# Kernel tuning notes

Measured on AMD Instinct MI355X. Metric: run time of the kernel, lower is better.

The kernel has to match this reference:

```python
import jax, jax.numpy as jnp
import numpy as np

GRID = 64            # volume_pixel per axis
VOX = 1.0 / GRID     # voxel_physical (unit-cube volume_physical)
CHUNK = 128          # gaussians per scan step


def _voxel_centers():
    # [V,3] centers of voxels of a unit cube, V = GRID**3
    c = (jnp.arange(GRID, dtype=jnp.float32) + 0.5) * VOX
    zz, yy, xx = jnp.meshgrid(c, c, c, indexing='ij')
    return jnp.stack([xx.ravel(), yy.ravel(), zz.ravel()], axis=-1)


def _quat_to_rotmat(q):
    # q: [N,4] (w,x,y,z), normalized -> [N,3,3]
    q = q / jnp.linalg.norm(q, axis=-1, keepdims=True)
    w, x, y, z = q[:, 0], q[:, 1], q[:, 2], q[:, 3]
    return jnp.stack([
        jnp.stack([1 - 2 * (y * y + z * z), 2 * (x * y - w * z), 2 * (x * z + w * y)], -1),
        jnp.stack([2 * (x * y + w * z), 1 - 2 * (x * x + z * z), 2 * (y * z - w * x)], -1),
        jnp.stack([2 * (x * z - w * y), 2 * (y * z + w * x), 1 - 2 * (x * x + y * y)], -1),
    ], axis=-2)


def _voxelize(means3D, densities, scales, rotations):
    N = means3D.shape[0]
    R = _quat_to_rotmat(rotations)                       # [N,3,3]
    inv_s2 = 1.0 / (scales * scales)                     # [N,3]
    # Sigma^{-1} = R diag(1/s^2) R^T
    Sinv = jnp.einsum('nij,nj,nkj->nik', R, inv_s2, R)   # [N,3,3]
    centers = _voxel_centers()                            # [V,3]
    n_chunks = N // CHUNK
    mu_c = means3D.reshape(n_chunks, CHUNK, 3)
    de_c = densities.reshape(n_chunks, CHUNK)
    Si_c = Sinv.reshape(n_chunks, CHUNK, 3, 3)

    def step(vol, xs):
        mu, dens, Si = xs
        d = centers[None, :, :] - mu[:, None, :]                 # [C,V,3]
        qf = jnp.einsum('cvi,cij,cvj->cv', d, Si, d)             # [C,V]
        vol = vol + jnp.sum(dens[:, None] * jnp.exp(-0.5 * qf), axis=0)
        return vol, None

    vol0 = jnp.zeros((GRID ** 3,), dtype=means3D.dtype)
    volume, _ = jax.lax.scan(step, vol0, (mu_c, de_c, Si_c))
    volume = volume.reshape(GRID, GRID, GRID)
    # screen-space-style radius: 3 sigma of the largest axis, in voxels
    radii = jnp.ceil(3.0 * jnp.max(scales, axis=-1) / VOX).astype(jnp.int32)
    return volume, radii


def setup_inputs() -> dict:
    key = jax.random.key(0)
    k1, k2, k3, k4 = jax.random.split(key, 4)
    N = 4096
    means3D = jax.random.uniform(k1, (N, 3), dtype=jnp.float32)                 # in unit cube
    densities = jax.random.uniform(k2, (N,), dtype=jnp.float32)
    scales = jax.random.uniform(k3, (N, 3), dtype=jnp.float32) * 0.05 + 0.01    # 0.6-3.8 voxels
    rotations = jax.random.normal(k4, (N, 4), dtype=jnp.float32)
    return {"means3D": means3D, "densities": densities, "scales": scales, "rotations": rotations}


def reference(means3D, densities, scales, rotations):
    return _voxelize(means3D, densities, scales, rotations)
```

## Files before the change

kernel.cpp:

```cpp
#include <hip/hip_runtime.h>

#define GRIDN 64
#define NVOX (GRIDN * GRIDN * GRIDN)
#define VOXF (1.0f / 64.0f)
#define QCUT 16.0f
#define EXPSCL (-0.72134752044f)
#define SKIPTH (QCUT * EXPSCL)

#define WS_CULLA 0
#define WS_CULLB (4 * 4096)
#define WS_REC   (8 * 4096)

__global__ __launch_bounds__(256) void prep_kernel(
    const float* __restrict__ means, const float* __restrict__ dens,
    const float* __restrict__ scales, const float* __restrict__ rots,
    float* __restrict__ ws, float* __restrict__ radii_out, int N)
{
    int i = blockIdx.x * 256 + threadIdx.x;
    if (i >= N) return;

    float qw = rots[i * 4 + 0], qx = rots[i * 4 + 1];
    float qy = rots[i * 4 + 2], qz = rots[i * 4 + 3];
    float inm = rsqrtf(qw * qw + qx * qx + qy * qy + qz * qz);
    qw *= inm; qx *= inm; qy *= inm; qz *= inm;
    float r00 = 1.f - 2.f * (qy * qy + qz * qz);
    float r01 = 2.f * (qx * qy - qw * qz);
    float r02 = 2.f * (qx * qz + qw * qy);
    float r10 = 2.f * (qx * qy + qw * qz);
    float r11 = 1.f - 2.f * (qx * qx + qz * qz);
    float r12 = 2.f * (qy * qz - qw * qx);
    float r20 = 2.f * (qx * qz - qw * qy);
    float r21 = 2.f * (qy * qz + qw * qx);
    float r22 = 1.f - 2.f * (qx * qx + qy * qy);

    float s0 = scales[i * 3 + 0], s1 = scales[i * 3 + 1], s2 = scales[i * 3 + 2];
    float v0 = s0 * s0, v1 = s1 * s1, v2 = s2 * s2;
    float i0 = 1.f / v0, i1 = 1.f / v1, i2 = 1.f / v2;

    float A = (r00 * r00 * i0 + r01 * r01 * i1 + r02 * r02 * i2) * EXPSCL;
    float B = (r10 * r10 * i0 + r11 * r11 * i1 + r12 * r12 * i2) * EXPSCL;
    float C = (r20 * r20 * i0 + r21 * r21 * i1 + r22 * r22 * i2) * EXPSCL;
    float D = (r00 * r10 * i0 + r01 * r11 * i1 + r02 * r12 * i2) * EXPSCL;
    float E = (r00 * r20 * i0 + r01 * r21 * i1 + r02 * r22 * i2) * EXPSCL;
    float F = (r10 * r20 * i0 + r11 * r21 * i1 + r12 * r22 * i2) * EXPSCL;

    float Cxx = r00 * r00 * v0 + r01 * r01 * v1 + r02 * r02 * v2;
    float Cyy = r10 * r10 * v0 + r11 * r11 * v1 + r12 * r12 * v2;
    float Czz = r20 * r20 * v0 + r21 * r21 * v1 + r22 * r22 * v2;

    float de = fmaxf(dens[i], 1e-30f);
    float qeff = fmaxf(QCUT + 2.0f * logf(de), 0.0f);
    float smax2 = fmaxf(v0, fmaxf(v1, v2));

    float mx = means[i * 3 + 0], my = means[i * 3 + 1], mz = means[i * 3 + 2];
    float4 ca; ca.x = mx; ca.y = my; ca.z = mz; ca.w = sqrtf(qeff * Cxx);
    float4 cb; cb.x = sqrtf(qeff * Cyy); cb.y = sqrtf(qeff * Czz);
    cb.z = qeff * smax2; cb.w = 0.f;
    ((float4*)(ws + WS_CULLA))[i] = ca;
    ((float4*)(ws + WS_CULLB))[i] = cb;

    float4* R = (float4*)(ws + WS_REC + (size_t)i * 16);
    float4 w0; w0.x = A; w0.y = B; w0.z = C; w0.w = 2.f * D;
    float4 w1; w1.x = 2.f * E; w1.y = 2.f * F; w1.z = -0.25f / A; w1.w = log2f(de);
    float4 w2; w2.x = mx; w2.y = my; w2.z = mz; w2.w = 0.f;
    R[0] = w0; R[1] = w1; R[2] = w2;

    float m = fmaxf(s0, fmaxf(s1, s2));
    radii_out[i] = ceilf(m * 3.0f * 64.0f);

    if (i == 0) {
        float4 zv; zv.x = 0.f; zv.y = 0.f; zv.z = 0.f; zv.w = 0.f;
        float4 d1; d1.x = 0.f; d1.y = 0.f; d1.z = 0.f; d1.w = -1e30f;
        float4* Dm = (float4*)(ws + WS_REC + (size_t)N * 16);
        Dm[0] = zv; Dm[1] = d1; Dm[2] = zv;
    }
}

__global__ __launch_bounds__(1024, 8) void vox_kernel(
    const float* __restrict__ ws, float* __restrict__ out, int N)
{
    __shared__ unsigned long long cmask[64];
    __shared__ int slist[3072];
    __shared__ float4 sreq[3][256];
    __shared__ float4 plds[16][64];

    const float* rec = ws + WS_REC;
    const int tid = threadIdx.x;
    const int lane = tid & 63, wave = tid >> 6;
    const int t = (blockIdx.x * 341) & 511;
    const int tX = t & 7, tY = (t >> 3) & 7, tZ = t >> 6;
    const int x0 = tX << 3;
    const int y = (tY << 3) + (lane & 7);
    const int z = (tZ << 3) + (lane >> 3);
    const float px = (x0 + 0.5f) * VOXF;
    const float py = (y + 0.5f) * VOXF;
    const float pz = (z + 0.5f) * VOXF;

    const float lox = (x0 + 0.5f) * VOXF,          hix = (x0 + 7.5f) * VOXF;
    const float loy = ((tY << 3) + 0.5f) * VOXF,   hiy = ((tY << 3) + 7.5f) * VOXF;
    const float loz = ((tZ << 3) + 0.5f) * VOXF,   hiz = ((tZ << 3) + 7.5f) * VOXF;

    const int nch = (N + 63) >> 6;
    #pragma unroll
    for (int k = 0; k < 4; ++k) {
        const int c = (k << 4) | wave;
        unsigned long long bal = 0ull;
        if (c < nch) {
            const int gi = (c << 6) + lane;
            const int gc = gi < N ? gi : N - 1;
            float4 ca = ((const float4*)(ws + WS_CULLA))[gc];
            float4 cb = ((const float4*)(ws + WS_CULLB))[gc];
            float cx = fminf(fmaxf(ca.x, lox), hix) - ca.x;
            float cy = fminf(fmaxf(ca.y, loy), hiy) - ca.y;
            float cz = fminf(fmaxf(ca.z, loz), hiz) - ca.z;
            float d2 = fmaf(cx, cx, fmaf(cy, cy, cz * cz));
            bool keep = (gi < N) && (d2 <= cb.z)
                && (ca.x + ca.w >= lox) && (ca.x - ca.w <= hix)
                && (ca.y + cb.x >= loy) && (ca.y - cb.x <= hiy)
                && (ca.z + cb.y >= loz) && (ca.z - cb.y <= hiz);
            bal = __ballot(keep);
        }
        if (lane == 0) cmask[c] = bal;
    }
    __syncthreads();

    unsigned long long mk = cmask[lane];
    int pc = __popcll(mk);
    int incl = pc;
    #pragma unroll
    for (int d = 1; d < 64; d <<= 1) {
        int t2 = __shfl_up(incl, d, 64);
        if (lane >= d) incl += t2;
    }
    const int excl = incl - pc;
    int cnt = __builtin_amdgcn_readlane(incl, 63);
    if (cnt > 3072) cnt = 3072;

    #pragma unroll
    for (int k = 0; k < 4; ++k) {
        const int c = (k << 4) | wave;
        unsigned long long mc = cmask[c];
        if (mc == 0ull) continue;
        int bse = __builtin_amdgcn_readlane(excl, c);
        if ((mc >> lane) & 1ull) {
            int pre = __popcll(mc & ((1ull << lane) - 1ull));
            int pos = bse + pre;
            if (pos < 3072) slist[pos] = (c << 6) + lane;
        }
    }
    int padend = ((cnt + 255) >> 8) << 8;
    if (padend > 3072) padend = 3072;
    for (int i = cnt + tid; i < padend; i += 1024) slist[i] = N;
    __syncthreads();

    float4 accL, accH;
    accL.x = accL.y = accL.z = accL.w = 0.f;
    accH = accL;

    for (int base = 0; base < padend; base += 256) {
        if (tid < 768) {
            const int part = tid >> 8, s = tid & 255;
            const int gi = slist[base + s];
            sreq[part][s] = ((const float4*)(rec + ((size_t)gi << 4)))[part];
        }
        __syncthreads();

        const int s0 = wave << 4;
        #pragma unroll 4
        for (int j = 0; j < 16; ++j) {
            float4 a0 = sreq[0][s0 + j];
            float4 a1 = sreq[1][s0 + j];
            float4 a2 = sreq[2][s0 + j];
            float dy = py - a2.y, dz = pz - a2.z;
            float tt  = fmaf(a1.y, dy, a0.z * dz);
            float qyz = fmaf(a0.y * dy, dy, fmaf(tt, dz, a1.w));
            float gx  = fmaf(a0.w, dy, a1.x * dz);
            float qmx = fmaf(gx * gx, a1.z, qyz);
            if (!__all(qmx < SKIPTH)) {
                float dx0 = px - a2.x;
                float dx1 = dx0 + VOXF,        dx2 = dx0 + 2.f * VOXF;
                float dx3 = dx0 + 3.f * VOXF,  dx4 = dx0 + 4.f * VOXF;
                float dx5 = dx0 + 5.f * VOXF,  dx6 = dx0 + 6.f * VOXF;
                float dx7 = dx0 + 7.f * VOXF;
                accL.x += __builtin_amdgcn_exp2f(fmaf(dx0, fmaf(a0.x, dx0, gx), qyz));
                accL.y += __builtin_amdgcn_exp2f(fmaf(dx1, fmaf(a0.x, dx1, gx), qyz));
                accL.z += __builtin_amdgcn_exp2f(fmaf(dx2, fmaf(a0.x, dx2, gx), qyz));
                accL.w += __builtin_amdgcn_exp2f(fmaf(dx3, fmaf(a0.x, dx3, gx), qyz));
                accH.x += __builtin_amdgcn_exp2f(fmaf(dx4, fmaf(a0.x, dx4, gx), qyz));
                accH.y += __builtin_amdgcn_exp2f(fmaf(dx5, fmaf(a0.x, dx5, gx), qyz));
                accH.z += __builtin_amdgcn_exp2f(fmaf(dx6, fmaf(a0.x, dx6, gx), qyz));
                accH.w += __builtin_amdgcn_exp2f(fmaf(dx7, fmaf(a0.x, dx7, gx), qyz));
            }
        }
        __syncthreads();
    }

    const int v = (z << 12) + (y << 6) + x0;

    plds[wave][lane] = accL;
    __syncthreads();
    if (wave == 0) {
        float4 r = plds[0][lane];
        #pragma unroll
        for (int w = 1; w < 16; ++w) {
            float4 p = plds[w][lane];
            r.x += p.x; r.y += p.y; r.z += p.z; r.w += p.w;
        }
        *(float4*)&out[v] = r;
    }
    __syncthreads();
    plds[wave][lane] = accH;
    __syncthreads();
    if (wave == 0) {
        float4 r = plds[0][lane];
        #pragma unroll
        for (int w = 1; w < 16; ++w) {
            float4 p = plds[w][lane];
            r.x += p.x; r.y += p.y; r.z += p.z; r.w += p.w;
        }
        *(float4*)&out[v + 4] = r;
    }
}

extern "C" void kernel_launch(void* const* d_in, const int* in_sizes, int n_in,
                              void* d_out, int out_size, void* d_ws, size_t ws_size,
                              hipStream_t stream)
{
    const float* means  = (const float*)d_in[0];
    const float* dens   = (const float*)d_in[1];
    const float* scales = (const float*)d_in[2];
    const float* rots   = (const float*)d_in[3];
    float* out = (float*)d_out;
    float* ws  = (float*)d_ws;
    const int N = in_sizes[1];

    prep_kernel<<<(N + 255) / 256, 256, 0, stream>>>(means, dens, scales, rots,
                                                     ws, out + NVOX, N);
    vox_kernel<<<512, 1024, 0, stream>>>(ws, out, N);
}
```

Measured before the change: 27.60 us.

## Fuse Gaussian preprocessing into voxel kernel, recomputing cull and quadric params per block

Drops the separate prep kernel and its workspace. Each block recomputes each Gaussian's culling bounds from the raw inputs during the cull phase, and rebuilds the quadric coefficients for the surviving Gaussians when staging them into shared memory. Radii output is written by the first 16 blocks. This removes one kernel launch and a global round trip. The cost is redundant per-block math: all 4096 cull parameter sets are recomputed in each of 512 blocks, and the staging of each 256-Gaussian batch now runs on 256 threads instead of 768.

```diff
diff --git a/kernel.cpp b/kernel.cpp
--- a/kernel.cpp
+++ b/kernel.cpp
@@ -7,84 +7,45 @@
 #define EXPSCL (-0.72134752044f)
 #define SKIPTH (QCUT * EXPSCL)
 
-#define WS_CULLA 0
-#define WS_CULLB (4 * 4096)
-#define WS_REC   (8 * 4096)
-
-__global__ __launch_bounds__(256) void prep_kernel(
+
+#define CULL_PARAMS(gc_, mx_, my_, mz_, rx_, ry_, rz_, sph_) do {              \
+    float qw = rots[(gc_) * 4 + 0], qx = rots[(gc_) * 4 + 1];                  \
+    float qy = rots[(gc_) * 4 + 2], qz = rots[(gc_) * 4 + 3];                  \
+    float inm = rsqrtf(qw * qw + qx * qx + qy * qy + qz * qz);                 \
+    qw *= inm; qx *= inm; qy *= inm; qz *= inm;                                \
+    float r00 = 1.f - 2.f * (qy * qy + qz * qz);                               \
+    float r01 = 2.f * (qx * qy - qw * qz);                                     \
+    float r02 = 2.f * (qx * qz + qw * qy);                                     \
+    float r10 = 2.f * (qx * qy + qw * qz);                                     \
+    float r11 = 1.f - 2.f * (qx * qx + qz * qz);                               \
+    float r12 = 2.f * (qy * qz - qw * qx);                                     \
+    float r20 = 2.f * (qx * qz - qw * qy);                                     \
+    float r21 = 2.f * (qy * qz + qw * qx);                                     \
+    float r22 = 1.f - 2.f * (qx * qx + qy * qy);                               \
+    float s0 = scales[(gc_) * 3 + 0], s1 = scales[(gc_) * 3 + 1];              \
+    float s2 = scales[(gc_) * 3 + 2];                                          \
+    float v0 = s0 * s0, v1 = s1 * s1, v2 = s2 * s2;                            \
+    float Cxx = r00 * r00 * v0 + r01 * r01 * v1 + r02 * r02 * v2;              \
+    float Cyy = r10 * r10 * v0 + r11 * r11 * v1 + r12 * r12 * v2;              \
+    float Czz = r20 * r20 * v0 + r21 * r21 * v1 + r22 * r22 * v2;              \
+    float de = fmaxf(dens[gc_], 1e-30f);                                       \
+    float qeff = fmaxf(QCUT + 2.0f * logf(de), 0.0f);                          \
+    mx_ = means[(gc_) * 3 + 0]; my_ = means[(gc_) * 3 + 1];                    \
+    mz_ = means[(gc_) * 3 + 2];                                                \
+    rx_ = sqrtf(qeff * Cxx); ry_ = sqrtf(qeff * Cyy); rz_ = sqrtf(qeff * Czz); \
+    sph_ = qeff * fmaxf(v0, fmaxf(v1, v2));                                    \
+} while (0)
+
+__global__ __launch_bounds__(1024, 8) void vox_kernel(
     const float* __restrict__ means, const float* __restrict__ dens,
     const float* __restrict__ scales, const float* __restrict__ rots,
-    float* __restrict__ ws, float* __restrict__ radii_out, int N)
-{
-    int i = blockIdx.x * 256 + threadIdx.x;
-    if (i >= N) return;
-
-    float qw = rots[i * 4 + 0], qx = rots[i * 4 + 1];
-    float qy = rots[i * 4 + 2], qz = rots[i * 4 + 3];
-    float inm = rsqrtf(qw * qw + qx * qx + qy * qy + qz * qz);
-    qw *= inm; qx *= inm; qy *= inm; qz *= inm;
-    float r00 = 1.f - 2.f * (qy * qy + qz * qz);
-    float r01 = 2.f * (qx * qy - qw * qz);
-    float r02 = 2.f * (qx * qz + qw * qy);
-    float r10 = 2.f * (qx * qy + qw * qz);
-    float r11 = 1.f - 2.f * (qx * qx + qz * qz);
-    float r12 = 2.f * (qy * qz - qw * qx);
-    float r20 = 2.f * (qx * qz - qw * qy);
-    float r21 = 2.f * (qy * qz + qw * qx);
-    float r22 = 1.f - 2.f * (qx * qx + qy * qy);
-
-    float s0 = scales[i * 3 + 0], s1 = scales[i * 3 + 1], s2 = scales[i * 3 + 2];
-    float v0 = s0 * s0, v1 = s1 * s1, v2 = s2 * s2;
-    float i0 = 1.f / v0, i1 = 1.f / v1, i2 = 1.f / v2;
-
-    float A = (r00 * r00 * i0 + r01 * r01 * i1 + r02 * r02 * i2) * EXPSCL;
-    float B = (r10 * r10 * i0 + r11 * r11 * i1 + r12 * r12 * i2) * EXPSCL;
-    float C = (r20 * r20 * i0 + r21 * r21 * i1 + r22 * r22 * i2) * EXPSCL;
-    float D = (r00 * r10 * i0 + r01 * r11 * i1 + r02 * r12 * i2) * EXPSCL;
-    float E = (r00 * r20 * i0 + r01 * r21 * i1 + r02 * r22 * i2) * EXPSCL;
-    float F = (r10 * r20 * i0 + r11 * r21 * i1 + r12 * r22 * i2) * EXPSCL;
-
-    float Cxx = r00 * r00 * v0 + r01 * r01 * v1 + r02 * r02 * v2;
-    float Cyy = r10 * r10 * v0 + r11 * r11 * v1 + r12 * r12 * v2;
-    float Czz = r20 * r20 * v0 + r21 * r21 * v1 + r22 * r22 * v2;
-
-    float de = fmaxf(dens[i], 1e-30f);
-    float qeff = fmaxf(QCUT + 2.0f * logf(de), 0.0f);
-    float smax2 = fmaxf(v0, fmaxf(v1, v2));
-
-    float mx = means[i * 3 + 0], my = means[i * 3 + 1], mz = means[i * 3 + 2];
-    float4 ca; ca.x = mx; ca.y = my; ca.z = mz; ca.w = sqrtf(qeff * Cxx);
-    float4 cb; cb.x = sqrtf(qeff * Cyy); cb.y = sqrtf(qeff * Czz);
-    cb.z = qeff * smax2; cb.w = 0.f;
-    ((float4*)(ws + WS_CULLA))[i] = ca;
-    ((float4*)(ws + WS_CULLB))[i] = cb;
-
-    float4* R = (float4*)(ws + WS_REC + (size_t)i * 16);
-    float4 w0; w0.x = A; w0.y = B; w0.z = C; w0.w = 2.f * D;
-    float4 w1; w1.x = 2.f * E; w1.y = 2.f * F; w1.z = -0.25f / A; w1.w = log2f(de);
-    float4 w2; w2.x = mx; w2.y = my; w2.z = mz; w2.w = 0.f;
-    R[0] = w0; R[1] = w1; R[2] = w2;
-
-    float m = fmaxf(s0, fmaxf(s1, s2));
-    radii_out[i] = ceilf(m * 3.0f * 64.0f);
-
-    if (i == 0) {
-        float4 zv; zv.x = 0.f; zv.y = 0.f; zv.z = 0.f; zv.w = 0.f;
-        float4 d1; d1.x = 0.f; d1.y = 0.f; d1.z = 0.f; d1.w = -1e30f;
-        float4* Dm = (float4*)(ws + WS_REC + (size_t)N * 16);
-        Dm[0] = zv; Dm[1] = d1; Dm[2] = zv;
-    }
-}
-
-__global__ __launch_bounds__(1024, 8) void vox_kernel(
-    const float* __restrict__ ws, float* __restrict__ out, int N)
+    float* __restrict__ out, int N)
 {
     __shared__ unsigned long long cmask[64];
     __shared__ int slist[3072];
     __shared__ float4 sreq[3][256];
     __shared__ float4 plds[16][64];
 
-    const float* rec = ws + WS_REC;
     const int tid = threadIdx.x;
     const int lane = tid & 63, wave = tid >> 6;
     const int t = (blockIdx.x * 341) & 511;
@@ -100,6 +61,15 @@
     const float loy = ((tY << 3) + 0.5f) * VOXF,   hiy = ((tY << 3) + 7.5f) * VOXF;
     const float loz = ((tZ << 3) + 0.5f) * VOXF,   hiz = ((tZ << 3) + 7.5f) * VOXF;
 
+    if (blockIdx.x < 16 && tid < 256) {
+        const int gi = (blockIdx.x << 8) + tid;
+        if (gi < N) {
+            float s0 = scales[gi * 3 + 0], s1 = scales[gi * 3 + 1];
+            float s2 = scales[gi * 3 + 2];
+            out[NVOX + gi] = ceilf(fmaxf(s0, fmaxf(s1, s2)) * 3.0f * 64.0f);
+        }
+    }
+
     const int nch = (N + 63) >> 6;
     #pragma unroll
     for (int k = 0; k < 4; ++k) {
@@ -108,16 +78,16 @@
         if (c < nch) {
             const int gi = (c << 6) + lane;
             const int gc = gi < N ? gi : N - 1;
-            float4 ca = ((const float4*)(ws + WS_CULLA))[gc];
-            float4 cb = ((const float4*)(ws + WS_CULLB))[gc];
-            float cx = fminf(fmaxf(ca.x, lox), hix) - ca.x;
-            float cy = fminf(fmaxf(ca.y, loy), hiy) - ca.y;
-            float cz = fminf(fmaxf(ca.z, loz), hiz) - ca.z;
+            float mx, my, mz, rx, ry, rz, sph;
+            CULL_PARAMS(gc, mx, my, mz, rx, ry, rz, sph);
+            float cx = fminf(fmaxf(mx, lox), hix) - mx;
+            float cy = fminf(fmaxf(my, loy), hiy) - my;
+            float cz = fminf(fmaxf(mz, loz), hiz) - mz;
             float d2 = fmaf(cx, cx, fmaf(cy, cy, cz * cz));
-            bool keep = (gi < N) && (d2 <= cb.z)
-                && (ca.x + ca.w >= lox) && (ca.x - ca.w <= hix)
-                && (ca.y + cb.x >= loy) && (ca.y - cb.x <= hiy)
-                && (ca.z + cb.y >= loz) && (ca.z - cb.y <= hiz);
+            bool keep = (gi < N) && (d2 <= sph)
+                && (mx + rx >= lox) && (mx - rx <= hix)
+                && (my + ry >= loy) && (my - ry <= hiy)
+                && (mz + rz >= loz) && (mz - rz <= hiz);
             bal = __ballot(keep);
         }
         if (lane == 0) cmask[c] = bal;
@@ -158,19 +128,52 @@
     accH = accL;
 
     for (int base = 0; base < padend; base += 256) {
-        if (tid < 768) {
-            const int part = tid >> 8, s = tid & 255;
-            const int gi = slist[base + s];
-            sreq[part][s] = ((const float4*)(rec + ((size_t)gi << 4)))[part];
+        if (tid < 256) {
+            const int gi = slist[base + tid];
+            float4 w0, w1, w2;
+            if (gi < N) {
+                float qw = rots[gi * 4 + 0], qx = rots[gi * 4 + 1];
+                float qy = rots[gi * 4 + 2], qz = rots[gi * 4 + 3];
+                float inm = rsqrtf(qw * qw + qx * qx + qy * qy + qz * qz);
+                qw *= inm; qx *= inm; qy *= inm; qz *= inm;
+                float r00 = 1.f - 2.f * (qy * qy + qz * qz);
+                float r01 = 2.f * (qx * qy - qw * qz);
+                float r02 = 2.f * (qx * qz + qw * qy);
+                float r10 = 2.f * (qx * qy + qw * qz);
+                float r11 = 1.f - 2.f * (qx * qx + qz * qz);
+                float r12 = 2.f * (qy * qz - qw * qx);
+                float r20 = 2.f * (qx * qz - qw * qy);
+                float r21 = 2.f * (qy * qz + qw * qx);
+                float r22 = 1.f - 2.f * (qx * qx + qy * qy);
+                float s0 = scales[gi * 3 + 0], s1 = scales[gi * 3 + 1];
+                float s2 = scales[gi * 3 + 2];
+                float i0 = 1.f / (s0 * s0), i1 = 1.f / (s1 * s1), i2 = 1.f / (s2 * s2);
+                float A = (r00 * r00 * i0 + r01 * r01 * i1 + r02 * r02 * i2) * EXPSCL;
+                float B = (r10 * r10 * i0 + r11 * r11 * i1 + r12 * r12 * i2) * EXPSCL;
+                float C = (r20 * r20 * i0 + r21 * r21 * i1 + r22 * r22 * i2) * EXPSCL;
+                float D = (r00 * r10 * i0 + r01 * r11 * i1 + r02 * r12 * i2) * EXPSCL;
+                float E = (r00 * r20 * i0 + r01 * r21 * i1 + r02 * r22 * i2) * EXPSCL;
+                float F = (r10 * r20 * i0 + r11 * r21 * i1 + r12 * r22 * i2) * EXPSCL;
+                float de = fmaxf(dens[gi], 1e-30f);
+                w0.x = A; w0.y = B; w0.z = C; w0.w = 2.f * D;
+                w1.x = 2.f * E; w1.y = 2.f * F; w1.z = -0.25f / A; w1.w = log2f(de);
+                w2.x = means[gi * 3 + 0]; w2.y = means[gi * 3 + 1];
+                w2.z = means[gi * 3 + 2]; w2.w = 0.f;
+            } else {
+                w0.x = w0.y = w0.z = w0.w = 0.f;
+                w1.x = w1.y = w1.z = 0.f; w1.w = -1e30f;
+                w2.x = w2.y = w2.z = w2.w = 0.f;
+            }
+            sreq[0][tid] = w0; sreq[1][tid] = w1; sreq[2][tid] = w2;
         }
         __syncthreads();
 
-        const int s0 = wave << 4;
+        const int s0i = wave << 4;
         #pragma unroll 4
         for (int j = 0; j < 16; ++j) {
-            float4 a0 = sreq[0][s0 + j];
-            float4 a1 = sreq[1][s0 + j];
-            float4 a2 = sreq[2][s0 + j];
+            float4 a0 = sreq[0][s0i + j];
+            float4 a1 = sreq[1][s0i + j];
+            float4 a2 = sreq[2][s0i + j];
             float dy = py - a2.y, dz = pz - a2.z;
             float tt  = fmaf(a1.y, dy, a0.z * dz);
             float qyz = fmaf(a0.y * dy, dy, fmaf(tt, dz, a1.w));
@@ -231,10 +234,7 @@
     const float* scales = (const float*)d_in[2];
     const float* rots   = (const float*)d_in[3];
     float* out = (float*)d_out;
-    float* ws  = (float*)d_ws;
     const int N = in_sizes[1];
 
-    prep_kernel<<<(N + 255) / 256, 256, 0, stream>>>(means, dens, scales, rots,
-                                                     ws, out + NVOX, N);
-    vox_kernel<<<512, 1024, 0, stream>>>(ws, out, N);
+    vox_kernel<<<512, 1024, 0, stream>>>(means, dens, scales, rots, out, N);
 }
```

Measured after the change: 29.44 us. +6.7%, slower.

## Give each wave a contiguous gaussian slice with scalar-indexed global loads

Applied to the files above, without the earlier changes.

Drops the shared-memory staging of gaussian records and the two block barriers per 256-record batch. Each wave now takes its own contiguous slice of the culled list, broadcasts indices with readlane and loads records directly from global memory (uniform addresses, likely scalar loads), unrolled four at a time. This removes the block-wide synchronization and LDS traffic, but adds global and cache load latency per record and can leave waves with unequal work.

```diff
diff --git a/kernel.cpp b/kernel.cpp
--- a/kernel.cpp
+++ b/kernel.cpp
@@ -76,12 +76,34 @@
     }
 }
 
+#define BODY8(v0_, v1_, v2_) do {                                             \
+    float dy = py - v2_.y, dz = pz - v2_.z;                                   \
+    float tt  = fmaf(v1_.y, dy, v0_.z * dz);                                  \
+    float qyz = fmaf(v0_.y * dy, dy, fmaf(tt, dz, v1_.w));                    \
+    float gx  = fmaf(v0_.w, dy, v1_.x * dz);                                  \
+    float qmx = fmaf(gx * gx, v1_.z, qyz);        \
+    if (!__all(qmx < SKIPTH)) {                                               \
+        float dx0 = px - v2_.x;                                               \
+        float dx1 = dx0 + VOXF,        dx2 = dx0 + 2.f * VOXF;                \
+        float dx3 = dx0 + 3.f * VOXF,  dx4 = dx0 + 4.f * VOXF;                \
+        float dx5 = dx0 + 5.f * VOXF,  dx6 = dx0 + 6.f * VOXF;                \
+        float dx7 = dx0 + 7.f * VOXF;                                         \
+        accL.x += __builtin_amdgcn_exp2f(fmaf(dx0, fmaf(v0_.x, dx0, gx), qyz));\
+        accL.y += __builtin_amdgcn_exp2f(fmaf(dx1, fmaf(v0_.x, dx1, gx), qyz));\
+        accL.z += __builtin_amdgcn_exp2f(fmaf(dx2, fmaf(v0_.x, dx2, gx), qyz));\
+        accL.w += __builtin_amdgcn_exp2f(fmaf(dx3, fmaf(v0_.x, dx3, gx), qyz));\
+        accH.x += __builtin_amdgcn_exp2f(fmaf(dx4, fmaf(v0_.x, dx4, gx), qyz));\
+        accH.y += __builtin_amdgcn_exp2f(fmaf(dx5, fmaf(v0_.x, dx5, gx), qyz));\
+        accH.z += __builtin_amdgcn_exp2f(fmaf(dx6, fmaf(v0_.x, dx6, gx), qyz));\
+        accH.w += __builtin_amdgcn_exp2f(fmaf(dx7, fmaf(v0_.x, dx7, gx), qyz));\
+    }                                                                         \
+} while (0)
+
 __global__ __launch_bounds__(1024, 8) void vox_kernel(
     const float* __restrict__ ws, float* __restrict__ out, int N)
 {
     __shared__ unsigned long long cmask[64];
     __shared__ int slist[3072];
-    __shared__ float4 sreq[3][256];
     __shared__ float4 plds[16][64];
 
     const float* rec = ws + WS_REC;
@@ -148,8 +170,10 @@
             if (pos < 3072) slist[pos] = (c << 6) + lane;
         }
     }
-    int padend = ((cnt + 255) >> 8) << 8;
-    if (padend > 3072) padend = 3072;
+
+    int L = (((cnt + 63) >> 6) + 0) << 2;
+    if (L << 4 > 3072) L = 192;
+    const int padend = L << 4;
     for (int i = cnt + tid; i < padend; i += 1024) slist[i] = N;
     __syncthreads();
 
@@ -157,42 +181,29 @@
     accL.x = accL.y = accL.z = accL.w = 0.f;
     accH = accL;
 
-    for (int base = 0; base < padend; base += 256) {
-        if (tid < 768) {
-            const int part = tid >> 8, s = tid & 255;
-            const int gi = slist[base + s];
-            sreq[part][s] = ((const float4*)(rec + ((size_t)gi << 4)))[part];
-        }
-        __syncthreads();
-
-        const int s0 = wave << 4;
-        #pragma unroll 4
-        for (int j = 0; j < 16; ++j) {
-            float4 a0 = sreq[0][s0 + j];
-            float4 a1 = sreq[1][s0 + j];
-            float4 a2 = sreq[2][s0 + j];
-            float dy = py - a2.y, dz = pz - a2.z;
-            float tt  = fmaf(a1.y, dy, a0.z * dz);
-            float qyz = fmaf(a0.y * dy, dy, fmaf(tt, dz, a1.w));
-            float gx  = fmaf(a0.w, dy, a1.x * dz);
-            float qmx = fmaf(gx * gx, a1.z, qyz);
-            if (!__all(qmx < SKIPTH)) {
-                float dx0 = px - a2.x;
-                float dx1 = dx0 + VOXF,        dx2 = dx0 + 2.f * VOXF;
-                float dx3 = dx0 + 3.f * VOXF,  dx4 = dx0 + 4.f * VOXF;
-                float dx5 = dx0 + 5.f * VOXF,  dx6 = dx0 + 6.f * VOXF;
-                float dx7 = dx0 + 7.f * VOXF;
-                accL.x += __builtin_amdgcn_exp2f(fmaf(dx0, fmaf(a0.x, dx0, gx), qyz));
-                accL.y += __builtin_amdgcn_exp2f(fmaf(dx1, fmaf(a0.x, dx1, gx), qyz));
-                accL.z += __builtin_amdgcn_exp2f(fmaf(dx2, fmaf(a0.x, dx2, gx), qyz));
-                accL.w += __builtin_amdgcn_exp2f(fmaf(dx3, fmaf(a0.x, dx3, gx), qyz));
-                accH.x += __builtin_amdgcn_exp2f(fmaf(dx4, fmaf(a0.x, dx4, gx), qyz));
-                accH.y += __builtin_amdgcn_exp2f(fmaf(dx5, fmaf(a0.x, dx5, gx), qyz));
-                accH.z += __builtin_amdgcn_exp2f(fmaf(dx6, fmaf(a0.x, dx6, gx), qyz));
-                accH.w += __builtin_amdgcn_exp2f(fmaf(dx7, fmaf(a0.x, dx7, gx), qyz));
-            }
-        }
-        __syncthreads();
+    const int beg = wave * L, end = beg + L;
+    for (int base = beg; base < end; base += 64) {
+        int src = base + lane;
+        int vidx = slist[src < padend ? src : padend - 1];
+        int m = end - base; if (m > 64) m = 64;
+        for (int j = 0; j < m; j += 4) {
+            int i0 = __builtin_amdgcn_readlane(vidx, j);
+            int i1 = __builtin_amdgcn_readlane(vidx, j + 1);
+            int i2 = __builtin_amdgcn_readlane(vidx, j + 2);
+            int i3 = __builtin_amdgcn_readlane(vidx, j + 3);
+            const float4* P0 = (const float4*)(rec + ((size_t)i0 << 4));
+            const float4* P1 = (const float4*)(rec + ((size_t)i1 << 4));
+            const float4* P2 = (const float4*)(rec + ((size_t)i2 << 4));
+            const float4* P3 = (const float4*)(rec + ((size_t)i3 << 4));
+            float4 a0 = P0[0], a1 = P0[1], a2 = P0[2];
+            float4 b0 = P1[0], b1 = P1[1], b2 = P1[2];
+            float4 c0 = P2[0], c1 = P2[1], c2 = P2[2];
+            float4 d0 = P3[0], d1 = P3[1], d2 = P3[2];
+            BODY8(a0, a1, a2);
+            BODY8(b0, b1, b2);
+            BODY8(c0, c1, c2);
+            BODY8(d0, d1, d2);
+        }
     }
 
     const int v = (z << 12) + (y << 6) + x0;
```

After: 27.63 us. Within noise of the previous version (+0.1%).
